# Performance work log

Hardware: AMD Instinct MI355X
Metric: run time of the kernel (lower is better)

The kernel has to match this reference:

```python
import jax, jax.numpy as jnp
import numpy as np

B, T, V, P, C = 1024, 6, 100, 20, 3
PC_RANGE = (-15.0, -30.0, -2.0, 15.0, 30.0, 2.0)
MAP_THRESH = 0.5
LANE_BOUND_CLS_IDX = 2
DIS_THRESH = 1.0
LOSS_WEIGHT = 1.0
MASK_VAL = 1e6


def _segments_intersect(s1, e1, s2, e2):
    # all args [..., 2]; standard 2D segment intersection via parametric solve
    d1 = e1 - s1
    d2 = e2 - s2
    det = d1[..., 0] * d2[..., 1] - d1[..., 1] * d2[..., 0]
    det_mask = det != 0
    det_safe = jnp.where(det_mask, det, jnp.ones_like(det))
    delta = s2 - s1
    t = (delta[..., 0] * d2[..., 1] - delta[..., 1] * d2[..., 0]) / det_safe
    u = (delta[..., 0] * d1[..., 1] - delta[..., 1] * d1[..., 0]) / det_safe
    return det_mask & (t >= 0) & (t <= 1) & (u >= 0) & (u <= 1)


def _plan_map_bound_loss(pred, target, dis_thresh):
    # pred: [B,T,2] future deltas; target: [B,V,P,2] lane boundary polylines
    pred = jnp.cumsum(pred, axis=-2)                                   # [B,T,2] traj points
    b, t, _ = pred.shape
    _, v, p, _ = target.shape
    starts = jnp.concatenate(
        [jnp.zeros((b, 1, 2), pred.dtype), pred[:, :-1, :]], axis=1)   # [B,T,2]

    # nearest map instance per trajectory point
    dist = jnp.linalg.norm(
        pred[:, :, None, None, :] - target[:, None, :, :, :], axis=-1)  # [B,T,V,P]
    dmin = dist.min(axis=-1)                                            # [B,T,V]
    min_inst = jnp.argmin(dmin, axis=-1)                                # [B,T]
    min_bd = target[jnp.arange(b)[:, None], min_inst]                   # [B,T,P,2]

    # ego segment (start->end) vs boundary segments of nearest instance
    inter = _segments_intersect(
        starts[:, :, None, :], pred[:, :, None, :],
        min_bd[:, :, :-1, :], min_bd[:, :, 1:, :])                      # [B,T,P-1]
    intersect_mask = inter.any(axis=-1)                                 # [B,T]

    # min distance to any map point (flattened over V*P)
    flat = target.reshape(b, v * p, 2)
    dist2 = jnp.linalg.norm(pred[:, :, None, :] - flat[:, None, :, :], axis=-1)  # [B,T,V*P]
    min_idx = jnp.argmin(dist2, axis=-1)                                # [B,T]
    min_dist = jnp.take_along_axis(dist2, min_idx[..., None], axis=-1)[..., 0]   # [B,T]

    loss = jnp.where(min_dist > dis_thresh,
                     jnp.zeros_like(min_dist), dis_thresh - min_dist)   # [B,T]

    # zero the suffix from the earliest intersecting timestep per batch
    ts = jnp.arange(t)
    first_t = jnp.where(intersect_mask, ts[None, :], t).min(axis=1)     # [B]
    loss = jnp.where(ts[None, :] >= first_t[:, None], jnp.zeros_like(loss), loss)
    return loss


def setup_inputs() -> dict:
    key = jax.random.key(0)
    k1, k2, k3 = jax.random.split(key, 3)
    ego_fut_preds = jax.random.normal(k1, (B, T, 2), dtype=jnp.float32)
    lane_preds = jax.random.uniform(k2, (B, V, P, 2), dtype=jnp.float32)
    lane_score_preds = jax.random.uniform(k3, (B, V, C), dtype=jnp.float32)
    return {"ego_fut_preds": ego_fut_preds, "lane_preds": lane_preds,
            "lane_score_preds": lane_score_preds}


def reference(ego_fut_preds, lane_preds, lane_score_preds):
    # denormalize lane coords into pc_range, mask non-boundary instances
    not_bound = lane_score_preds[..., LANE_BOUND_CLS_IDX] < MAP_THRESH   # [B,V]
    scale = jnp.array([PC_RANGE[3] - PC_RANGE[0], PC_RANGE[4] - PC_RANGE[1]],
                      dtype=lane_preds.dtype)
    offset = jnp.array([PC_RANGE[0], PC_RANGE[1]], dtype=lane_preds.dtype)
    lane_bound = lane_preds * scale + offset                             # [B,V,P,2]
    lane_bound = jnp.where(not_bound[:, :, None, None], MASK_VAL, lane_bound)
    loss = _plan_map_bound_loss(ego_fut_preds, lane_bound, DIS_THRESH)   # [B,T]
    return LOSS_WEIGHT * loss.mean()
```

## Files before the change

### kernel.cpp

```cpp
#include <hip/hip_runtime.h>
#include <math.h>

constexpr int Bn = 1024, Tn = 6, Vn = 100, Pn = 20, Cn = 3;
constexpr int NT = 256;
constexpr int NF4 = Vn * Pn * 2 / 4;
constexpr unsigned TAG = 0x13579BDFu;

__global__ __launch_bounds__(NT) void pmbl_fused(
    const float* __restrict__ ego,
    const float* __restrict__ lane,
    const float* __restrict__ score,
    float* __restrict__ out,
    unsigned long long* __restrict__ slots)
{
    const int b = blockIdx.x;
    const int tid = threadIdx.x;

    __shared__ int smask[Vn];
    __shared__ unsigned long long red[NT / 64][Tn];
    __shared__ int interMask;
    __shared__ double sm[NT / 64];

    const float4* lp4 = reinterpret_cast<const float4*>(
        lane + (size_t)b * (Vn * Pn * 2));
    float4 q0 = lp4[tid];
    float4 q1 = lp4[tid + NT];
    float4 q2 = lp4[tid + 2 * NT];
    const bool has3 = tid < NF4 - 3 * NT;
    float4 q3 = has3 ? lp4[tid + 3 * NT] : make_float4(0.f, 0.f, 0.f, 0.f);

    float scv = 0.f;
    if (tid < Vn) scv = score[(size_t)b * (Vn * Cn) + tid * Cn + 2];

    float px[Tn], py[Tn], sx[Tn], sy[Tn];
    {
        const float* e = ego + (size_t)b * (Tn * 2);
        float cx = 0.f, cy = 0.f;
        #pragma unroll
        for (int t = 0; t < Tn; ++t) {
            sx[t] = cx; sy[t] = cy;
            cx += e[2 * t];
            cy += e[2 * t + 1];
            px[t] = cx; py[t] = cy;
        }
    }

    if (tid < Vn) smask[tid] = (scv < 0.5f) ? 1 : 0;
    if (tid == 0) interMask = 0;
    __syncthreads();

    float best[Tn]; int bidx[Tn];
    #pragma unroll
    for (int t = 0; t < Tn; ++t) { best[t] = __builtin_inff(); bidx[t] = 0; }

    auto process = [&](int f, float4 q) {
        const int v = f / 10;
        const bool nb = smask[v] != 0;
        const float x0 = nb ? 1e6f : fmaf(q.x, 30.f, -15.f);
        const float y0 = nb ? 1e6f : fmaf(q.y, 60.f, -30.f);
        const float x1 = nb ? 1e6f : fmaf(q.z, 30.f, -15.f);
        const float y1 = nb ? 1e6f : fmaf(q.w, 60.f, -30.f);
        const int p0 = 2 * f, p1 = 2 * f + 1;
        #pragma unroll
        for (int t = 0; t < Tn; ++t) {
            float dx0 = px[t] - x0, dy0 = py[t] - y0;
            float s0 = dx0 * dx0 + dy0 * dy0;
            float dx1 = px[t] - x1, dy1 = py[t] - y1;
            float s1 = dx1 * dx1 + dy1 * dy1;
            if (s0 < best[t]) { best[t] = s0; bidx[t] = p0; }
            if (s1 < best[t]) { best[t] = s1; bidx[t] = p1; }
        }
    };

    process(tid, q0);
    process(tid + NT, q1);
    process(tid + 2 * NT, q2);
    if (has3) process(tid + 3 * NT, q3);

    unsigned long long pk[Tn];
    #pragma unroll
    for (int t = 0; t < Tn; ++t)
        pk[t] = (((unsigned long long)__float_as_uint(best[t])) << 32)
                | (unsigned)bidx[t];

    #pragma unroll
    for (int off = 32; off > 0; off >>= 1) {
        #pragma unroll
        for (int t = 0; t < Tn; ++t) {
            unsigned long long o = __shfl_xor(pk[t], off);
            pk[t] = (o < pk[t]) ? o : pk[t];
        }
    }
    if ((tid & 63) == 0) {
        #pragma unroll
        for (int t = 0; t < Tn; ++t) red[tid >> 6][t] = pk[t];
    }
    __syncthreads();

    unsigned long long comb[Tn];
    #pragma unroll
    for (int t = 0; t < Tn; ++t) {
        unsigned long long m = red[0][t];
        #pragma unroll
        for (int w = 1; w < NT / 64; ++w) {
            unsigned long long c = red[w][t];
            m = (c < m) ? c : m;
        }
        comb[t] = m;
    }

    if (tid < Tn * (Pn - 1)) {
        const int t = tid / (Pn - 1);
        const int s = tid % (Pn - 1);
        const int vt = (int)(comb[t] & 0xffffffffu) / Pn;
        const bool nb = smask[vt] != 0;
        const float* lp = lane + ((size_t)b * Vn + vt) * (Pn * 2);
        float ax = nb ? 1e6f : fmaf(lp[2 * s + 0], 30.f, -15.f);
        float ay = nb ? 1e6f : fmaf(lp[2 * s + 1], 60.f, -30.f);
        float bx = nb ? 1e6f : fmaf(lp[2 * s + 2], 30.f, -15.f);
        float by = nb ? 1e6f : fmaf(lp[2 * s + 3], 60.f, -30.f);
        float d1x = px[t] - sx[t], d1y = py[t] - sy[t];
        float d2x = bx - ax, d2y = by - ay;
        float det = d1x * d2y - d1y * d2x;
        if (det != 0.f) {
            float dx = ax - sx[t], dy = ay - sy[t];
            float tt = (dx * d2y - dy * d2x) / det;
            float uu = (dx * d1y - dy * d1x) / det;
            if (tt >= 0.f && tt <= 1.f && uu >= 0.f && uu <= 1.f)
                atomicOr(&interMask, 1 << t);
        }
    }
    __syncthreads();

    if (tid == 0) {
        const int im = interMask;
        int first_t = Tn;
        #pragma unroll
        for (int t = Tn - 1; t >= 0; --t)
            if ((im >> t) & 1) first_t = t;
        float sum = 0.f;
        for (int t = 0; t < first_t; ++t) {
            float d = sqrtf(__uint_as_float((unsigned)(comb[t] >> 32)));
            sum += (d > 1.f) ? 0.f : (1.f - d);
        }
        unsigned long long v = (((unsigned long long)TAG) << 32)
                             | (unsigned long long)__float_as_uint(sum);
        __hip_atomic_store(&slots[b], v, __ATOMIC_RELAXED,
                           __HIP_MEMORY_SCOPE_AGENT);
    }

    if (b == 0) {
        double s = 0.0;
        for (int j = tid; j < Bn; j += NT) {
            unsigned long long v = __hip_atomic_load(
                &slots[j], __ATOMIC_RELAXED, __HIP_MEMORY_SCOPE_AGENT);
            while ((unsigned)(v >> 32) != TAG) {
                __builtin_amdgcn_s_sleep(8);
                v = __hip_atomic_load(&slots[j], __ATOMIC_RELAXED,
                                      __HIP_MEMORY_SCOPE_AGENT);
            }
            s += (double)__uint_as_float((unsigned)(v & 0xffffffffu));
        }
        #pragma unroll
        for (int off = 32; off > 0; off >>= 1) s += __shfl_xor(s, off);
        if ((tid & 63) == 0) sm[tid >> 6] = s;
        __syncthreads();
        if (tid == 0) {
            double tot = 0.0;
            #pragma unroll
            for (int w = 0; w < NT / 64; ++w) tot += sm[w];
            out[0] = (float)(tot / (double)(Bn * Tn));
        }
    }
}

extern "C" void kernel_launch(void* const* d_in, const int* in_sizes, int n_in,
                              void* d_out, int out_size, void* d_ws, size_t ws_size,
                              hipStream_t stream) {
    const float* ego   = (const float*)d_in[0];
    const float* lane  = (const float*)d_in[1];
    const float* score = (const float*)d_in[2];
    float* out = (float*)d_out;
    unsigned long long* slots = (unsigned long long*)d_ws;

    pmbl_fused<<<Bn, NT, 0, stream>>>(ego, lane, score, out, slots);
}
```

Measured before the change: 14.28 us.

## Replace packed argmin reduction with float min reduction plus index rescan

The per-timestep nearest-point search now tracks only the minimum squared distance with fminf, and reduces it with 32-bit float shuffles instead of 64-bit packed (distance,index) compares. The argmin index is recovered afterwards: threads whose local minimum equals the block minimum recompute the distances and atomicMin the matching index into shared memory. This cuts register pressure and halves shuffle traffic, at the cost of an extra barrier, a rescan and shared atomics. It also switches the squared distance to an fma form, which could change rounding ties slightly.

Result: no change. 14.15 us, median of 2 (-0.9%).

```diff
diff --git a/kernel.cpp b/kernel.cpp
--- a/kernel.cpp
+++ b/kernel.cpp
@@ -5,6 +5,21 @@
 constexpr int NT = 256;
 constexpr int NF4 = Vn * Pn * 2 / 4;
 constexpr unsigned TAG = 0x13579BDFu;
+constexpr unsigned IDX_NONE = 0xffffffffu;
+
+__device__ __forceinline__ float sqd(float px, float py, float x, float y) {
+    float dx = px - x, dy = py - y;
+    return fmaf(dx, dx, dy * dy);
+}
+
+__device__ __forceinline__ void coords(float4 q, bool nb,
+                                       float& x0, float& y0,
+                                       float& x1, float& y1) {
+    x0 = nb ? 1e6f : fmaf(q.x, 30.f, -15.f);
+    y0 = nb ? 1e6f : fmaf(q.y, 60.f, -30.f);
+    x1 = nb ? 1e6f : fmaf(q.z, 30.f, -15.f);
+    y1 = nb ? 1e6f : fmaf(q.w, 60.f, -30.f);
+}
 
 __global__ __launch_bounds__(NT) void pmbl_fused(
     const float* __restrict__ ego,
@@ -17,9 +32,14 @@
     const int tid = threadIdx.x;
 
     __shared__ int smask[Vn];
-    __shared__ unsigned long long red[NT / 64][Tn];
+    __shared__ float redf[NT / 64][Tn];
+    __shared__ float Mt[Tn];
+    __shared__ unsigned idxMin[Tn];
     __shared__ int interMask;
     __shared__ double sm[NT / 64];
+
+    float scv = 0.f;
+    if (tid < Vn) scv = score[(size_t)b * (Vn * Cn) + tid * Cn + 2];
 
     const float4* lp4 = reinterpret_cast<const float4*>(
         lane + (size_t)b * (Vn * Pn * 2));
@@ -29,9 +49,6 @@
     const bool has3 = tid < NF4 - 3 * NT;
     float4 q3 = has3 ? lp4[tid + 3 * NT] : make_float4(0.f, 0.f, 0.f, 0.f);
 
-    float scv = 0.f;
-    if (tid < Vn) scv = score[(size_t)b * (Vn * Cn) + tid * Cn + 2];
-
     float px[Tn], py[Tn], sx[Tn], sy[Tn];
     {
         const float* e = ego + (size_t)b * (Tn * 2);
@@ -46,29 +63,24 @@
     }
 
     if (tid < Vn) smask[tid] = (scv < 0.5f) ? 1 : 0;
+    if (tid < Tn) idxMin[tid] = IDX_NONE;
     if (tid == 0) interMask = 0;
     __syncthreads();
 
-    float best[Tn]; int bidx[Tn];
-    #pragma unroll
-    for (int t = 0; t < Tn; ++t) { best[t] = __builtin_inff(); bidx[t] = 0; }
+    float best[Tn];
+    #pragma unroll
+    for (int t = 0; t < Tn; ++t) best[t] = __builtin_inff();
 
     auto process = [&](int f, float4 q) {
         const int v = f / 10;
         const bool nb = smask[v] != 0;
-        const float x0 = nb ? 1e6f : fmaf(q.x, 30.f, -15.f);
-        const float y0 = nb ? 1e6f : fmaf(q.y, 60.f, -30.f);
-        const float x1 = nb ? 1e6f : fmaf(q.z, 30.f, -15.f);
-        const float y1 = nb ? 1e6f : fmaf(q.w, 60.f, -30.f);
-        const int p0 = 2 * f, p1 = 2 * f + 1;
+        float x0, y0, x1, y1;
+        coords(q, nb, x0, y0, x1, y1);
         #pragma unroll
         for (int t = 0; t < Tn; ++t) {
-            float dx0 = px[t] - x0, dy0 = py[t] - y0;
-            float s0 = dx0 * dx0 + dy0 * dy0;
-            float dx1 = px[t] - x1, dy1 = py[t] - y1;
-            float s1 = dx1 * dx1 + dy1 * dy1;
-            if (s0 < best[t]) { best[t] = s0; bidx[t] = p0; }
-            if (s1 < best[t]) { best[t] = s1; bidx[t] = p1; }
+            float s0 = sqd(px[t], py[t], x0, y0);
+            float s1 = sqd(px[t], py[t], x1, y1);
+            best[t] = fminf(best[t], fminf(s0, s1));
         }
     };
 
@@ -77,42 +89,56 @@
     process(tid + 2 * NT, q2);
     if (has3) process(tid + 3 * NT, q3);
 
-    unsigned long long pk[Tn];
-    #pragma unroll
-    for (int t = 0; t < Tn; ++t)
-        pk[t] = (((unsigned long long)__float_as_uint(best[t])) << 32)
-                | (unsigned)bidx[t];
-
+    float w[Tn];
+    #pragma unroll
+    for (int t = 0; t < Tn; ++t) w[t] = best[t];
     #pragma unroll
     for (int off = 32; off > 0; off >>= 1) {
         #pragma unroll
-        for (int t = 0; t < Tn; ++t) {
-            unsigned long long o = __shfl_xor(pk[t], off);
-            pk[t] = (o < pk[t]) ? o : pk[t];
-        }
+        for (int t = 0; t < Tn; ++t)
+            w[t] = fminf(w[t], __shfl_xor(w[t], off));
     }
     if ((tid & 63) == 0) {
         #pragma unroll
-        for (int t = 0; t < Tn; ++t) red[tid >> 6][t] = pk[t];
-    }
-    __syncthreads();
-
-    unsigned long long comb[Tn];
+        for (int t = 0; t < Tn; ++t) redf[tid >> 6][t] = w[t];
+    }
+    __syncthreads();
+
+    if (tid < Tn) {
+        float m = redf[0][tid];
+        #pragma unroll
+        for (int wv = 1; wv < NT / 64; ++wv) m = fminf(m, redf[wv][tid]);
+        Mt[tid] = m;
+    }
+    __syncthreads();
+
+    auto rescan4 = [&](int f, float4 q, float ptx, float pty, float tgt,
+                       unsigned* slot) {
+        const int v = f / 10;
+        const bool nb = smask[v] != 0;
+        float x0, y0, x1, y1;
+        coords(q, nb, x0, y0, x1, y1);
+        if (sqd(ptx, pty, x0, y0) == tgt) atomicMin(slot, 2u * f);
+        if (sqd(ptx, pty, x1, y1) == tgt) atomicMin(slot, 2u * f + 1u);
+    };
     #pragma unroll
     for (int t = 0; t < Tn; ++t) {
-        unsigned long long m = red[0][t];
-        #pragma unroll
-        for (int w = 1; w < NT / 64; ++w) {
-            unsigned long long c = red[w][t];
-            m = (c < m) ? c : m;
-        }
-        comb[t] = m;
-    }
+        if (best[t] == Mt[t]) {
+            rescan4(tid,          q0, px[t], py[t], Mt[t], &idxMin[t]);
+            rescan4(tid + NT,     q1, px[t], py[t], Mt[t], &idxMin[t]);
+            rescan4(tid + 2 * NT, q2, px[t], py[t], Mt[t], &idxMin[t]);
+            if (has3)
+                rescan4(tid + 3 * NT, q3, px[t], py[t], Mt[t], &idxMin[t]);
+        }
+    }
+    __syncthreads();
 
     if (tid < Tn * (Pn - 1)) {
         const int t = tid / (Pn - 1);
         const int s = tid % (Pn - 1);
-        const int vt = (int)(comb[t] & 0xffffffffu) / Pn;
+        unsigned idx = idxMin[t];
+        unsigned vtu = idx / (unsigned)Pn;
+        const int vt = (vtu < (unsigned)Vn) ? (int)vtu : 0;
         const bool nb = smask[vt] != 0;
         const float* lp = lane + ((size_t)b * Vn + vt) * (Pn * 2);
         float ax = nb ? 1e6f : fmaf(lp[2 * s + 0], 30.f, -15.f);
@@ -140,7 +166,7 @@
             if ((im >> t) & 1) first_t = t;
         float sum = 0.f;
         for (int t = 0; t < first_t; ++t) {
-            float d = sqrtf(__uint_as_float((unsigned)(comb[t] >> 32)));
+            float d = sqrtf(Mt[t]);
             sum += (d > 1.f) ? 0.f : (1.f - d);
         }
         unsigned long long v = (((unsigned long long)TAG) << 32)
@@ -168,7 +194,7 @@
         if (tid == 0) {
             double tot = 0.0;
             #pragma unroll
-            for (int w = 0; w < NT / 64; ++w) tot += sm[w];
+            for (int wv = 0; wv < NT / 64; ++wv) tot += sm[wv];
             out[0] = (float)(tot / (double)(Bn * Tn));
         }
     }
```

## Split per-batch nearest-point search across four blocks and add tail kernel

Applied to the files above, without the earlier changes.

The single fused kernel becomes two. The first splits each batch's 100 lane instances into 4 parts, each handled by a 128-thread block, and writes packed per-part min/argmin values to workspace. A second kernel combines the parts, runs the segment-intersection test, and does the cross-block spin-wait final reduction with a shorter sleep. The goal is more parallelism and less per-thread serial work. The cost is an extra kernel launch plus a global round-trip for the partial results.

Result: slower. 20.55 us (+43.9%).

```diff
diff --git a/kernel.cpp b/kernel.cpp
--- a/kernel.cpp
+++ b/kernel.cpp
@@ -2,80 +2,87 @@
 #include <math.h>
 
 constexpr int Bn = 1024, Tn = 6, Vn = 100, Pn = 20, Cn = 3;
-constexpr int NT = 256;
-constexpr int NF4 = Vn * Pn * 2 / 4;
+constexpr int PARTS = 4;
+constexpr int F4PP = 250;
+constexpr int LPP = Vn / PARTS;
+constexpr int NT1 = 128;
+constexpr int NT2 = 128;
 constexpr unsigned TAG = 0x13579BDFu;
 
-__global__ __launch_bounds__(NT) void pmbl_fused(
+__device__ __forceinline__ float sqd(float px, float py, float x, float y) {
+    float dx = px - x, dy = py - y;
+    return fmaf(dx, dx, dy * dy);
+}
+
+__device__ __forceinline__ void coords(float4 q, bool nb,
+                                       float& x0, float& y0,
+                                       float& x1, float& y1) {
+    x0 = nb ? 1e6f : fmaf(q.x, 30.f, -15.f);
+    y0 = nb ? 1e6f : fmaf(q.y, 60.f, -30.f);
+    x1 = nb ? 1e6f : fmaf(q.z, 30.f, -15.f);
+    y1 = nb ? 1e6f : fmaf(q.w, 60.f, -30.f);
+}
+
+__global__ __launch_bounds__(NT1) void pmbl_part(
     const float* __restrict__ ego,
     const float* __restrict__ lane,
     const float* __restrict__ score,
-    float* __restrict__ out,
-    unsigned long long* __restrict__ slots)
+    unsigned long long* __restrict__ partial)
 {
-    const int b = blockIdx.x;
+    const int bid = blockIdx.x;
+    const int b = bid >> 2, part = bid & 3;
     const int tid = threadIdx.x;
 
-    __shared__ int smask[Vn];
-    __shared__ unsigned long long red[NT / 64][Tn];
-    __shared__ int interMask;
-    __shared__ double sm[NT / 64];
+    __shared__ int smL[LPP];
+    __shared__ unsigned long long red[2][Tn];
 
     const float4* lp4 = reinterpret_cast<const float4*>(
         lane + (size_t)b * (Vn * Pn * 2));
-    float4 q0 = lp4[tid];
-    float4 q1 = lp4[tid + NT];
-    float4 q2 = lp4[tid + 2 * NT];
-    const bool has3 = tid < NF4 - 3 * NT;
-    float4 q3 = has3 ? lp4[tid + 3 * NT] : make_float4(0.f, 0.f, 0.f, 0.f);
+    const int fbase = part * F4PP;
+    float4 q0 = lp4[fbase + tid];
+    const bool has1 = tid < F4PP - NT1;
+    float4 q1 = has1 ? lp4[fbase + tid + NT1] : make_float4(0.f,0.f,0.f,0.f);
 
     float scv = 0.f;
-    if (tid < Vn) scv = score[(size_t)b * (Vn * Cn) + tid * Cn + 2];
-
-    float px[Tn], py[Tn], sx[Tn], sy[Tn];
+    if (tid < LPP)
+        scv = score[(size_t)b * (Vn * Cn) + (part * LPP + tid) * Cn + 2];
+
+    float px[Tn], py[Tn];
     {
         const float* e = ego + (size_t)b * (Tn * 2);
         float cx = 0.f, cy = 0.f;
         #pragma unroll
         for (int t = 0; t < Tn; ++t) {
-            sx[t] = cx; sy[t] = cy;
             cx += e[2 * t];
             cy += e[2 * t + 1];
             px[t] = cx; py[t] = cy;
         }
     }
 
-    if (tid < Vn) smask[tid] = (scv < 0.5f) ? 1 : 0;
-    if (tid == 0) interMask = 0;
+    if (tid < LPP) smL[tid] = (scv < 0.5f) ? 1 : 0;
     __syncthreads();
 
     float best[Tn]; int bidx[Tn];
     #pragma unroll
     for (int t = 0; t < Tn; ++t) { best[t] = __builtin_inff(); bidx[t] = 0; }
 
-    auto process = [&](int f, float4 q) {
-        const int v = f / 10;
-        const bool nb = smask[v] != 0;
-        const float x0 = nb ? 1e6f : fmaf(q.x, 30.f, -15.f);
-        const float y0 = nb ? 1e6f : fmaf(q.y, 60.f, -30.f);
-        const float x1 = nb ? 1e6f : fmaf(q.z, 30.f, -15.f);
-        const float y1 = nb ? 1e6f : fmaf(q.w, 60.f, -30.f);
-        const int p0 = 2 * f, p1 = 2 * f + 1;
-        #pragma unroll
-        for (int t = 0; t < Tn; ++t) {
-            float dx0 = px[t] - x0, dy0 = py[t] - y0;
-            float s0 = dx0 * dx0 + dy0 * dy0;
-            float dx1 = px[t] - x1, dy1 = py[t] - y1;
-            float s1 = dx1 * dx1 + dy1 * dy1;
+    auto process = [&](int fl, float4 q) {
+        const int v = fl / 10;
+        const bool nb = smL[v] != 0;
+        float x0, y0, x1, y1;
+        coords(q, nb, x0, y0, x1, y1);
+        const int p0 = 2 * (fbase + fl), p1 = p0 + 1;
+        #pragma unroll
+        for (int t = 0; t < Tn; ++t) {
+            float s0 = sqd(px[t], py[t], x0, y0);
+            float s1 = sqd(px[t], py[t], x1, y1);
             if (s0 < best[t]) { best[t] = s0; bidx[t] = p0; }
             if (s1 < best[t]) { best[t] = s1; bidx[t] = p1; }
         }
     };
 
     process(tid, q0);
-    process(tid + NT, q1);
-    process(tid + 2 * NT, q2);
-    if (has3) process(tid + 3 * NT, q3);
+    if (has1) process(tid + NT1, q1);
 
     unsigned long long pk[Tn];
     #pragma unroll
@@ -97,23 +104,60 @@
     }
     __syncthreads();
 
-    unsigned long long comb[Tn];
-    #pragma unroll
-    for (int t = 0; t < Tn; ++t) {
-        unsigned long long m = red[0][t];
-        #pragma unroll
-        for (int w = 1; w < NT / 64; ++w) {
-            unsigned long long c = red[w][t];
+    if (tid < Tn) {
+        unsigned long long a = red[0][tid], c = red[1][tid];
+        partial[((size_t)b * PARTS + part) * Tn + tid] = (c < a) ? c : a;
+    }
+}
+
+__global__ __launch_bounds__(NT2) void pmbl_tail(
+    const float* __restrict__ ego,
+    const float* __restrict__ lane,
+    const float* __restrict__ score,
+    float* __restrict__ out,
+    const unsigned long long* __restrict__ partial,
+    unsigned long long* __restrict__ slots)
+{
+    const int b = blockIdx.x;
+    const int tid = threadIdx.x;
+
+    __shared__ unsigned long long comb6[Tn];
+    __shared__ int interMask;
+    __shared__ double sm[NT2 / 64];
+
+    if (tid == 0) interMask = 0;
+    if (tid < Tn) {
+        const unsigned long long* p = partial + (size_t)b * PARTS * Tn;
+        unsigned long long m = p[tid];
+        #pragma unroll
+        for (int q = 1; q < PARTS; ++q) {
+            unsigned long long c = p[q * Tn + tid];
             m = (c < m) ? c : m;
         }
-        comb[t] = m;
-    }
+        comb6[tid] = m;
+    }
+
+    float px[Tn], py[Tn], sx[Tn], sy[Tn];
+    {
+        const float* e = ego + (size_t)b * (Tn * 2);
+        float cx = 0.f, cy = 0.f;
+        #pragma unroll
+        for (int t = 0; t < Tn; ++t) {
+            sx[t] = cx; sy[t] = cy;
+            cx += e[2 * t];
+            cy += e[2 * t + 1];
+            px[t] = cx; py[t] = cy;
+        }
+    }
+    __syncthreads();
 
     if (tid < Tn * (Pn - 1)) {
         const int t = tid / (Pn - 1);
         const int s = tid % (Pn - 1);
-        const int vt = (int)(comb[t] & 0xffffffffu) / Pn;
-        const bool nb = smask[vt] != 0;
+        unsigned idx = (unsigned)(comb6[t] & 0xffffffffu);
+        unsigned vtu = idx / (unsigned)Pn;
+        const int vt = (vtu < (unsigned)Vn) ? (int)vtu : 0;
+        const bool nb = score[(size_t)b * (Vn * Cn) + vt * Cn + 2] < 0.5f;
         const float* lp = lane + ((size_t)b * Vn + vt) * (Pn * 2);
         float ax = nb ? 1e6f : fmaf(lp[2 * s + 0], 30.f, -15.f);
         float ay = nb ? 1e6f : fmaf(lp[2 * s + 1], 60.f, -30.f);
@@ -140,7 +184,7 @@
             if ((im >> t) & 1) first_t = t;
         float sum = 0.f;
         for (int t = 0; t < first_t; ++t) {
-            float d = sqrtf(__uint_as_float((unsigned)(comb[t] >> 32)));
+            float d = sqrtf(__uint_as_float((unsigned)(comb6[t] >> 32)));
             sum += (d > 1.f) ? 0.f : (1.f - d);
         }
         unsigned long long v = (((unsigned long long)TAG) << 32)
@@ -151,11 +195,11 @@
 
     if (b == 0) {
         double s = 0.0;
-        for (int j = tid; j < Bn; j += NT) {
+        for (int j = tid; j < Bn; j += NT2) {
             unsigned long long v = __hip_atomic_load(
                 &slots[j], __ATOMIC_RELAXED, __HIP_MEMORY_SCOPE_AGENT);
             while ((unsigned)(v >> 32) != TAG) {
-                __builtin_amdgcn_s_sleep(8);
+                __builtin_amdgcn_s_sleep(2);
                 v = __hip_atomic_load(&slots[j], __ATOMIC_RELAXED,
                                       __HIP_MEMORY_SCOPE_AGENT);
             }
@@ -168,7 +212,7 @@
         if (tid == 0) {
             double tot = 0.0;
             #pragma unroll
-            for (int w = 0; w < NT / 64; ++w) tot += sm[w];
+            for (int w = 0; w < NT2 / 64; ++w) tot += sm[w];
             out[0] = (float)(tot / (double)(Bn * Tn));
         }
     }
@@ -181,7 +225,9 @@
     const float* lane  = (const float*)d_in[1];
     const float* score = (const float*)d_in[2];
     float* out = (float*)d_out;
-    unsigned long long* slots = (unsigned long long*)d_ws;
-
-    pmbl_fused<<<Bn, NT, 0, stream>>>(ego, lane, score, out, slots);
-}
+    unsigned long long* partial = (unsigned long long*)d_ws;
+    unsigned long long* slots   = partial + (size_t)Bn * PARTS * Tn;
+
+    pmbl_part<<<Bn * PARTS, NT1, 0, stream>>>(ego, lane, score, partial);
+    pmbl_tail<<<Bn, NT2, 0, stream>>>(ego, lane, score, out, partial, slots);
+}
```

## Process two batches per 512-thread block and halve grid size

Applied to the files above, without the earlier changes.

Each block now has 512 threads and handles two batch elements (b and b+512). Both elements' lane data is loaded up front, then each is processed in turn. This halves the grid size and gives each thread two float4 loads per batch instead of four. It also changes the distance computation to use an fma and shortens the spin sleep in the final reduction block. The cost is that the two batches are processed one after the other inside each block, and the larger block needs more barriers and register pressure under launch_bounds(512,4).

Result: slower. 26.26 us (+84.0%).

```diff
diff --git a/kernel.cpp b/kernel.cpp
--- a/kernel.cpp
+++ b/kernel.cpp
@@ -2,160 +2,168 @@
 #include <math.h>
 
 constexpr int Bn = 1024, Tn = 6, Vn = 100, Pn = 20, Cn = 3;
-constexpr int NT = 256;
+constexpr int NT = 512;
+constexpr int NBLK = 512;
 constexpr int NF4 = Vn * Pn * 2 / 4;
 constexpr unsigned TAG = 0x13579BDFu;
 
-__global__ __launch_bounds__(NT) void pmbl_fused(
+__global__ __launch_bounds__(NT, 4) void pmbl_fused(
     const float* __restrict__ ego,
     const float* __restrict__ lane,
     const float* __restrict__ score,
     float* __restrict__ out,
     unsigned long long* __restrict__ slots)
 {
-    const int b = blockIdx.x;
     const int tid = threadIdx.x;
+    const int bA = blockIdx.x;
+    const int bB = bA + NBLK;
 
-    __shared__ int smask[Vn];
+    __shared__ int smA[Vn], smB[Vn];
     __shared__ unsigned long long red[NT / 64][Tn];
-    __shared__ int interMask;
+    __shared__ int imA, imB;
     __shared__ double sm[NT / 64];
 
-    const float4* lp4 = reinterpret_cast<const float4*>(
-        lane + (size_t)b * (Vn * Pn * 2));
-    float4 q0 = lp4[tid];
-    float4 q1 = lp4[tid + NT];
-    float4 q2 = lp4[tid + 2 * NT];
-    const bool has3 = tid < NF4 - 3 * NT;
-    float4 q3 = has3 ? lp4[tid + 3 * NT] : make_float4(0.f, 0.f, 0.f, 0.f);
+    const float4* lpA = reinterpret_cast<const float4*>(
+        lane + (size_t)bA * (Vn * Pn * 2));
+    const float4* lpB = reinterpret_cast<const float4*>(
+        lane + (size_t)bB * (Vn * Pn * 2));
+    const bool has1 = tid < NF4 - NT;
+    float4 qA0 = lpA[tid];
+    float4 qA1 = has1 ? lpA[tid + NT] : make_float4(0.f, 0.f, 0.f, 0.f);
+    float4 qB0 = lpB[tid];
+    float4 qB1 = has1 ? lpB[tid + NT] : make_float4(0.f, 0.f, 0.f, 0.f);
 
-    float scv = 0.f;
-    if (tid < Vn) scv = score[(size_t)b * (Vn * Cn) + tid * Cn + 2];
+    if (tid < Vn) {
+        smA[tid] = (score[(size_t)bA * (Vn * Cn) + tid * Cn + 2] < 0.5f) ? 1 : 0;
+        smB[tid] = (score[(size_t)bB * (Vn * Cn) + tid * Cn + 2] < 0.5f) ? 1 : 0;
+    }
+    if (tid == 0) { imA = 0; imB = 0; }
+    __syncthreads();
 
-    float px[Tn], py[Tn], sx[Tn], sy[Tn];
-    {
-        const float* e = ego + (size_t)b * (Tn * 2);
-        float cx = 0.f, cy = 0.f;
+    auto run = [&](int b, const float4* lp4, float4 q0, float4 q1,
+                   const int* smask, int* im) {
+        float px[Tn], py[Tn], sx[Tn], sy[Tn];
+        {
+            const float* e = ego + (size_t)b * (Tn * 2);
+            float cx = 0.f, cy = 0.f;
+            #pragma unroll
+            for (int t = 0; t < Tn; ++t) {
+                sx[t] = cx; sy[t] = cy;
+                cx += e[2 * t];
+                cy += e[2 * t + 1];
+                px[t] = cx; py[t] = cy;
+            }
+        }
+
+        float best[Tn]; int bidx[Tn];
+        #pragma unroll
+        for (int t = 0; t < Tn; ++t) { best[t] = __builtin_inff(); bidx[t] = 0; }
+
+        auto process = [&](int f, float4 q) {
+            const int v = f / 10;
+            const bool nb = smask[v] != 0;
+            const float x0 = nb ? 1e6f : fmaf(q.x, 30.f, -15.f);
+            const float y0 = nb ? 1e6f : fmaf(q.y, 60.f, -30.f);
+            const float x1 = nb ? 1e6f : fmaf(q.z, 30.f, -15.f);
+            const float y1 = nb ? 1e6f : fmaf(q.w, 60.f, -30.f);
+            const int p0 = 2 * f, p1 = 2 * f + 1;
+            #pragma unroll
+            for (int t = 0; t < Tn; ++t) {
+                float dx0 = px[t] - x0, dy0 = py[t] - y0;
+                float s0 = fmaf(dx0, dx0, dy0 * dy0);
+                float dx1 = px[t] - x1, dy1 = py[t] - y1;
+                float s1 = fmaf(dx1, dx1, dy1 * dy1);
+                if (s0 < best[t]) { best[t] = s0; bidx[t] = p0; }
+                if (s1 < best[t]) { best[t] = s1; bidx[t] = p1; }
+            }
+        };
+        process(tid, q0);
+        if (has1) process(tid + NT, q1);
+
+        unsigned long long pk[Tn];
+        #pragma unroll
+        for (int t = 0; t < Tn; ++t)
+            pk[t] = (((unsigned long long)__float_as_uint(best[t])) << 32)
+                    | (unsigned)bidx[t];
+        #pragma unroll
+        for (int off = 32; off > 0; off >>= 1) {
+            #pragma unroll
+            for (int t = 0; t < Tn; ++t) {
+                unsigned long long o = __shfl_xor(pk[t], off);
+                pk[t] = (o < pk[t]) ? o : pk[t];
+            }
+        }
+        if ((tid & 63) == 0) {
+            #pragma unroll
+            for (int t = 0; t < Tn; ++t) red[tid >> 6][t] = pk[t];
+        }
+        __syncthreads();
+
+        unsigned long long comb[Tn];
         #pragma unroll
         for (int t = 0; t < Tn; ++t) {
-            sx[t] = cx; sy[t] = cy;
-            cx += e[2 * t];
-            cy += e[2 * t + 1];
-            px[t] = cx; py[t] = cy;
+            unsigned long long m = red[0][t];
+            #pragma unroll
+            for (int w = 1; w < NT / 64; ++w) {
+                unsigned long long c = red[w][t];
+                m = (c < m) ? c : m;
+            }
+            comb[t] = m;
         }
-    }
 
-    if (tid < Vn) smask[tid] = (scv < 0.5f) ? 1 : 0;
-    if (tid == 0) interMask = 0;
-    __syncthreads();
+        if (tid < Tn * (Pn - 1)) {
+            const int t = tid / (Pn - 1);
+            const int s = tid % (Pn - 1);
+            const int vt = (int)(comb[t] & 0xffffffffu) / Pn;
+            const bool nb = smask[vt] != 0;
+            const float* lp = reinterpret_cast<const float*>(lp4) + vt * (Pn * 2);
+            float ax = nb ? 1e6f : fmaf(lp[2 * s + 0], 30.f, -15.f);
+            float ay = nb ? 1e6f : fmaf(lp[2 * s + 1], 60.f, -30.f);
+            float bx = nb ? 1e6f : fmaf(lp[2 * s + 2], 30.f, -15.f);
+            float by = nb ? 1e6f : fmaf(lp[2 * s + 3], 60.f, -30.f);
+            float d1x = px[t] - sx[t], d1y = py[t] - sy[t];
+            float d2x = bx - ax, d2y = by - ay;
+            float det = d1x * d2y - d1y * d2x;
+            if (det != 0.f) {
+                float dx = ax - sx[t], dy = ay - sy[t];
+                float tt = (dx * d2y - dy * d2x) / det;
+                float uu = (dx * d1y - dy * d1x) / det;
+                if (tt >= 0.f && tt <= 1.f && uu >= 0.f && uu <= 1.f)
+                    atomicOr(im, 1 << t);
+            }
+        }
+        __syncthreads();
 
-    float best[Tn]; int bidx[Tn];
-    #pragma unroll
-    for (int t = 0; t < Tn; ++t) { best[t] = __builtin_inff(); bidx[t] = 0; }
-
-    auto process = [&](int f, float4 q) {
-        const int v = f / 10;
-        const bool nb = smask[v] != 0;
-        const float x0 = nb ? 1e6f : fmaf(q.x, 30.f, -15.f);
-        const float y0 = nb ? 1e6f : fmaf(q.y, 60.f, -30.f);
-        const float x1 = nb ? 1e6f : fmaf(q.z, 30.f, -15.f);
-        const float y1 = nb ? 1e6f : fmaf(q.w, 60.f, -30.f);
-        const int p0 = 2 * f, p1 = 2 * f + 1;
-        #pragma unroll
-        for (int t = 0; t < Tn; ++t) {
-            float dx0 = px[t] - x0, dy0 = py[t] - y0;
-            float s0 = dx0 * dx0 + dy0 * dy0;
-            float dx1 = px[t] - x1, dy1 = py[t] - y1;
-            float s1 = dx1 * dx1 + dy1 * dy1;
-            if (s0 < best[t]) { best[t] = s0; bidx[t] = p0; }
-            if (s1 < best[t]) { best[t] = s1; bidx[t] = p1; }
+        if (tid == 0) {
+            const int m = *im;
+            int first_t = Tn;
+            #pragma unroll
+            for (int t = Tn - 1; t >= 0; --t)
+                if ((m >> t) & 1) first_t = t;
+            float sum = 0.f;
+            for (int t = 0; t < first_t; ++t) {
+                float d = sqrtf(__uint_as_float((unsigned)(comb[t] >> 32)));
+                sum += (d > 1.f) ? 0.f : (1.f - d);
+            }
+            unsigned long long v = (((unsigned long long)TAG) << 32)
+                                 | (unsigned long long)__float_as_uint(sum);
+            __hip_atomic_store(&slots[b], v, __ATOMIC_RELAXED,
+                               __HIP_MEMORY_SCOPE_AGENT);
         }
     };
 
-    process(tid, q0);
-    process(tid + NT, q1);
-    process(tid + 2 * NT, q2);
-    if (has3) process(tid + 3 * NT, q3);
+    run(bA, lpA, qA0, qA1, smA, &imA);
+    run(bB, lpB, qB0, qB1, smB, &imB);
 
-    unsigned long long pk[Tn];
-    #pragma unroll
-    for (int t = 0; t < Tn; ++t)
-        pk[t] = (((unsigned long long)__float_as_uint(best[t])) << 32)
-                | (unsigned)bidx[t];
-
-    #pragma unroll
-    for (int off = 32; off > 0; off >>= 1) {
+    if (blockIdx.x == 0) {
+        double s = 0.0;
         #pragma unroll
-        for (int t = 0; t < Tn; ++t) {
-            unsigned long long o = __shfl_xor(pk[t], off);
-            pk[t] = (o < pk[t]) ? o : pk[t];
-        }
-    }
-    if ((tid & 63) == 0) {
-        #pragma unroll
-        for (int t = 0; t < Tn; ++t) red[tid >> 6][t] = pk[t];
-    }
-    __syncthreads();
-
-    unsigned long long comb[Tn];
-    #pragma unroll
-    for (int t = 0; t < Tn; ++t) {
-        unsigned long long m = red[0][t];
-        #pragma unroll
-        for (int w = 1; w < NT / 64; ++w) {
-            unsigned long long c = red[w][t];
-            m = (c < m) ? c : m;
-        }
-        comb[t] = m;
-    }
-
-    if (tid < Tn * (Pn - 1)) {
-        const int t = tid / (Pn - 1);
-        const int s = tid % (Pn - 1);
-        const int vt = (int)(comb[t] & 0xffffffffu) / Pn;
-        const bool nb = smask[vt] != 0;
-        const float* lp = lane + ((size_t)b * Vn + vt) * (Pn * 2);
-        float ax = nb ? 1e6f : fmaf(lp[2 * s + 0], 30.f, -15.f);
-        float ay = nb ? 1e6f : fmaf(lp[2 * s + 1], 60.f, -30.f);
-        float bx = nb ? 1e6f : fmaf(lp[2 * s + 2], 30.f, -15.f);
-        float by = nb ? 1e6f : fmaf(lp[2 * s + 3], 60.f, -30.f);
-        float d1x = px[t] - sx[t], d1y = py[t] - sy[t];
-        float d2x = bx - ax, d2y = by - ay;
-        float det = d1x * d2y - d1y * d2x;
-        if (det != 0.f) {
-            float dx = ax - sx[t], dy = ay - sy[t];
-            float tt = (dx * d2y - dy * d2x) / det;
-            float uu = (dx * d1y - dy * d1x) / det;
-            if (tt >= 0.f && tt <= 1.f && uu >= 0.f && uu <= 1.f)
-                atomicOr(&interMask, 1 << t);
-        }
-    }
-    __syncthreads();
-
-    if (tid == 0) {
-        const int im = interMask;
-        int first_t = Tn;
-        #pragma unroll
-        for (int t = Tn - 1; t >= 0; --t)
-            if ((im >> t) & 1) first_t = t;
-        float sum = 0.f;
-        for (int t = 0; t < first_t; ++t) {
-            float d = sqrtf(__uint_as_float((unsigned)(comb[t] >> 32)));
-            sum += (d > 1.f) ? 0.f : (1.f - d);
-        }
-        unsigned long long v = (((unsigned long long)TAG) << 32)
-                             | (unsigned long long)__float_as_uint(sum);
-        __hip_atomic_store(&slots[b], v, __ATOMIC_RELAXED,
-                           __HIP_MEMORY_SCOPE_AGENT);
-    }
-
-    if (b == 0) {
-        double s = 0.0;
-        for (int j = tid; j < Bn; j += NT) {
+        for (int r = 0; r < Bn / NT; ++r) {
+            const int j = tid + r * NT;
             unsigned long long v = __hip_atomic_load(
                 &slots[j], __ATOMIC_RELAXED, __HIP_MEMORY_SCOPE_AGENT);
             while ((unsigned)(v >> 32) != TAG) {
-                __builtin_amdgcn_s_sleep(8);
+                __builtin_amdgcn_s_sleep(1);
                 v = __hip_atomic_load(&slots[j], __ATOMIC_RELAXED,
                                       __HIP_MEMORY_SCOPE_AGENT);
             }
@@ -183,5 +191,5 @@
     float* out = (float*)d_out;
     unsigned long long* slots = (unsigned long long*)d_ws;
 
-    pmbl_fused<<<Bn, NT, 0, stream>>>(ego, lane, score, out, slots);
+    pmbl_fused<<<NBLK, NT, 0, stream>>>(ego, lane, score, out, slots);
 }
```
